# Kernel tuning notes

Measured on AMD Instinct MI355X. Metric: run time of the kernel, lower is better.

The kernel has to match this reference:

```python
import jax, jax.numpy as jnp
import numpy as np

BATCH, SEQ, HIDDEN = 8, 2048, 2048
N_FREQS = SEQ // 2 + 1  # 1025


def setup_inputs() -> dict:
    key = jax.random.key(0)
    k_x, k_w, k_b = jax.random.split(key, 3)
    x = jax.random.normal(k_x, (BATCH, SEQ, HIDDEN), dtype=jnp.float32)
    # Params per __init__: gate init ones/zeros; Linear(hidden, hidden)
    gate_real = jnp.ones((N_FREQS, HIDDEN), dtype=jnp.float32)
    gate_imag = jnp.zeros((N_FREQS, HIDDEN), dtype=jnp.float32)
    bound = 1.0 / np.sqrt(HIDDEN)
    W = jax.random.uniform(k_w, (HIDDEN, HIDDEN), minval=-bound, maxval=bound, dtype=jnp.float32)
    b = jax.random.uniform(k_b, (HIDDEN,), minval=-bound, maxval=bound, dtype=jnp.float32)
    return {"x": x, "gate_real": gate_real, "gate_imag": gate_imag, "W": W, "b": b}


def reference(x, gate_real, gate_imag, W, b):
    # x: (batch, seq, hidden)
    seq_len = x.shape[1]
    x_fft = jnp.fft.rfft(x, axis=1)  # (batch, n_freqs, hidden) complex64
    n_freqs = x_fft.shape[1]
    gate = gate_real[:n_freqs] + 1j * gate_imag[:n_freqs]  # (n_freqs, hidden)
    x_fft = x_fft * gate
    y = jnp.fft.irfft(x_fft, n=seq_len, axis=1)  # (batch, seq, hidden) float32
    # out_proj: y @ W.T + b  (torch Linear convention, W: (out, in))
    out = jnp.einsum('bsh,oh->bso', y, W) + b
    return out
```

## Files before the change

### kernel.cpp

```cpp
#include <hip/hip_runtime.h>
#include <math.h>

typedef __attribute__((ext_vector_type(8))) short bf16x8;
typedef __attribute__((ext_vector_type(4))) float f32x4;

__device__ __forceinline__ unsigned short f2bf(float f) {
  unsigned int u = __float_as_uint(f);
  unsigned int r = (u + 0x7fffu + ((u >> 16) & 1u)) >> 16;
  return (unsigned short)r;
}
__device__ __forceinline__ unsigned int pack2bf(float a, float b) {
  return (unsigned int)f2bf(a) | ((unsigned int)f2bf(b) << 16);
}
__device__ __forceinline__ float bflo(unsigned int g) { return __uint_as_float(g << 16); }
__device__ __forceinline__ float bfhi(unsigned int g) { return __uint_as_float(g & 0xffff0000u); }

__device__ __forceinline__ void glds16(const void* gp, void* lp) {
  __builtin_amdgcn_global_load_lds(
      (const __attribute__((address_space(1))) void*)gp,
      (__attribute__((address_space(3))) void*)lp, 16, 0, 0);
}

__device__ __constant__ float CW16[16] = {
  1.0f, 0.9807852804032304f, 0.9238795325112867f, 0.8314696123025452f,
  0.7071067811865476f, 0.5555702330196022f, 0.3826834323650898f, 0.19509032201612828f,
  0.0f, -0.19509032201612828f, -0.3826834323650898f, -0.5555702330196022f,
  -0.7071067811865476f, -0.8314696123025452f, -0.9238795325112867f, -0.9807852804032304f};
__device__ __constant__ float SW16[16] = {
  0.0f, 0.19509032201612828f, 0.3826834323650898f, 0.5555702330196022f,
  0.7071067811865476f, 0.8314696123025452f, 0.9238795325112867f, 0.9807852804032304f,
  1.0f, 0.9807852804032304f, 0.9238795325112867f, 0.8314696123025452f,
  0.7071067811865476f, 0.5555702330196022f, 0.3826834323650898f, 0.19509032201612828f};
__device__ __constant__ int BR5[32] = {
  0,16,8,24,4,20,12,28,2,18,10,26,6,22,14,30,
  1,17,9,25,5,21,13,29,3,19,11,27,7,23,15,31};

__device__ __forceinline__ int bitrev6(int l) {
  return ((l&1)<<5)|((l&2)<<3)|((l&4)<<1)|((l&8)>>1)|((l&16)>>3)|((l&32)>>5);
}

__device__ __forceinline__ float hsin(float rev) { return __builtin_amdgcn_sinf(rev); }
__device__ __forceinline__ float hcos(float rev) { return __builtin_amdgcn_cosf(rev); }

__device__ __forceinline__ void fwd_core(float (&ur)[32], float (&ui)[32], const int lane) {
  #pragma unroll
  for (int s = 0; s < 6; ++s) {
    const int h = 32 >> s;
    const int j = lane & (h - 1);
    const float rev = (float)j * (0.5f / (float)h);
    const bool hi = (lane & h) != 0;
    const float c  = hi ? hcos(rev) : 1.0f;
    const float sv = hi ? hsin(rev) : 0.0f;
    const float sgn = hi ? -1.0f : 1.0f;
    #pragma unroll
    for (int r = 0; r < 32; ++r) {
      float pr = __shfl_xor(ur[r], h, 64);
      float pi = __shfl_xor(ui[r], h, 64);
      float tr = fmaf(sgn, ur[r], pr);
      float ti = fmaf(sgn, ui[r], pi);
      ur[r] = fmaf(ti, sv, tr * c);
      ui[r] = fmaf(-tr, sv, ti * c);
    }
  }
  const int kap = bitrev6(lane);
  #pragma unroll
  for (int j = 1; j < 32; ++j) {
    const float rev = (float)(j * kap) * (1.0f / 2048.0f);
    const float sn = hsin(rev), cs = hcos(rev);
    float t = ur[j] * cs + ui[j] * sn;
    ui[j] = ui[j] * cs - ur[j] * sn;
    ur[j] = t;
  }
  #pragma unroll
  for (int s = 0; s < 5; ++s) {
    const int h = 16 >> s;
    #pragma unroll
    for (int i = 0; i < 32; ++i) if (!(i & h)) {
      const int tw = (i & (h - 1)) * (16 / h);
      float dr = ur[i] - ur[i + h], di = ui[i] - ui[i + h];
      ur[i] += ur[i + h]; ui[i] += ui[i + h];
      ur[i + h] = dr * CW16[tw] + di * SW16[tw];
      ui[i + h] = di * CW16[tw] - dr * SW16[tw];
    }
  }
}

__device__ __forceinline__ void inv_core(float (&ur)[32], float (&ui)[32], const int lane) {
  const int kap = bitrev6(lane);
  #pragma unroll
  for (int s = 0; s < 5; ++s) {
    const int h = 1 << s;
    #pragma unroll
    for (int i = 0; i < 32; ++i) if (!(i & h)) {
      const int tw = (i & (h - 1)) * (16 / h);
      float tr2 = ur[i + h] * CW16[tw] - ui[i + h] * SW16[tw];
      float ti2 = ui[i + h] * CW16[tw] + ur[i + h] * SW16[tw];
      ur[i + h] = ur[i] - tr2; ui[i + h] = ui[i] - ti2;
      ur[i] += tr2; ui[i] += ti2;
    }
  }
  #pragma unroll
  for (int j = 1; j < 32; ++j) {
    const float rev = (float)(j * kap) * (1.0f / 2048.0f);
    const float sn = hsin(rev), cs = hcos(rev);
    float t = ur[j] * cs - ui[j] * sn;
    ui[j] = ui[j] * cs + ur[j] * sn;
    ur[j] = t;
  }
  #pragma unroll
  for (int s = 0; s < 6; ++s) {
    const int h = 1 << s;
    const int j = lane & (h - 1);
    const float rev = (float)j * (0.5f / (float)h);
    const bool hi = (lane & h) != 0;
    const float c  = hi ? hcos(rev) : 1.0f;
    const float sv = hi ? hsin(rev) : 0.0f;
    const float sgn = hi ? -1.0f : 1.0f;
    #pragma unroll
    for (int r = 0; r < 32; ++r) {
      float vr = fmaf(-ui[r], sv, ur[r] * c);
      float vi = fmaf(ur[r], sv, ui[r] * c);
      float pvr = __shfl_xor(vr, h, 64);
      float pvi = __shfl_xor(vi, h, 64);
      ur[r] = fmaf(sgn, vr, pvr);
      ui[r] = fmaf(sgn, vi, pvi);
    }
  }
}

__global__ __launch_bounds__(256) void gate_pack_k(const float* __restrict__ gr,
                                                   const float* __restrict__ gi,
                                                   unsigned int* __restrict__ gt) {
  __shared__ float tr[32][33];
  __shared__ float ti[32][33];
  const int t = threadIdx.x;
  const int k0 = blockIdx.x * 32, hb = blockIdx.y * 32;
  const int hx = t & 31, fr = t >> 5;
  #pragma unroll
  for (int p = 0; p < 4; ++p) {
    int ff = p * 8 + fr;
    int k = k0 + ff;
    int f = (k <= 1024) ? k : (2048 - k);
    float sg = (k <= 1024) ? 1.f : -1.f;
    tr[ff][hx] = gr[(size_t)f * 2048 + hb + hx] * (1.f / 2048.f);
    ti[ff][hx] = sg * gi[(size_t)f * 2048 + hb + hx] * (1.f / 2048.f);
  }
  __syncthreads();
  const int kk = t & 31, hr = t >> 5;
  #pragma unroll
  for (int p = 0; p < 4; ++p) {
    int hl = p * 8 + hr;
    float re = tr[kk][hl], im = ti[kk][hl];
    gt[(size_t)(hb + hl) * 2048 + k0 + kk] =
        (unsigned int)f2bf(re) | ((unsigned int)f2bf(im) << 16);
  }
}

__global__ __launch_bounds__(256) void gate_ab_k(const float* __restrict__ gr,
                                                 const float* __restrict__ gi,
                                                 uint2* __restrict__ ab) {
  __shared__ unsigned int uA[32][33];
  __shared__ unsigned int uB[32][33];
  const int t = threadIdx.x;
  const int k0 = blockIdx.x * 32, h0 = blockIdx.y * 32;
  const int c = t & 31, r = t >> 5;
  #pragma unroll
  for (int pp = 0; pp < 4; ++pp) {
    const int kk = pp * 8 + r;
    const int k = k0 + kk;
    const int h = h0 + c;
    const float gkr = gr[(size_t)k * 2048 + h];
    const float gki = gi[(size_t)k * 2048 + h];
    const float gcr = gr[(size_t)(1024 - k) * 2048 + h];
    const float gci = gi[(size_t)(1024 - k) * 2048 + h];
    const float inv = 1.0f / 1024.0f;
    float Ar, Ai, Br, Bi;
    if (k == 0) {
      Ar = (gkr + gcr) * 0.5f * inv; Ai = 0.f;
      Br = 0.f; Bi = (gkr - gcr) * 0.5f * inv;
    } else {
      const float rev = (float)k * (1.0f / 2048.0f);
      const float sn = hsin(rev), cs = hcos(rev);
      const float Sr = (gkr + gcr) * 0.5f, Si = (gki - gci) * 0.5f;
      const float Dr = (gkr - gcr) * 0.5f, Di = (gki + gci) * 0.5f;
      Ar = (Sr - sn * Dr) * inv; Ai = (Si - sn * Di) * inv;
      Br = (-cs * Di) * inv;     Bi = (cs * Dr) * inv;
    }
    uA[kk][c] = pack2bf(Ar, Ai);
    uB[kk][c] = pack2bf(Br, Bi);
  }
  __syncthreads();
  #pragma unroll
  for (int pp = 0; pp < 4; ++pp) {
    const int hh = pp * 8 + r;
    ab[(size_t)(h0 + hh) * 1024 + k0 + c] = make_uint2(uA[c][hh], uB[c][hh]);
  }
}

__global__ __launch_bounds__(256) void wconv_k(const float* __restrict__ W,
                                               unsigned short* __restrict__ Wb) {
  int i = blockIdx.x * 256 + threadIdx.x;
  float4 v = ((const float4*)W)[i];
  ushort4 o;
  o.x = f2bf(v.x); o.y = f2bf(v.y); o.z = f2bf(v.z); o.w = f2bf(v.w);
  ((ushort4*)Wb)[i] = o;
}

__global__ __launch_bounds__(256) void xtrans_k(const float* __restrict__ x,
                                                unsigned short* __restrict__ xT) {
  __shared__ float t[64][65];
  const int b = blockIdx.z;
  const int s0 = blockIdx.x * 64, h0 = blockIdx.y * 64;
  const float* xb = x + ((size_t)b * 2048) * 2048;
  unsigned short* xTb = xT + ((size_t)b * 2048) * 2048;
  const int c4 = (threadIdx.x & 15) * 4;
  const int r0 = threadIdx.x >> 4;
  #pragma unroll
  for (int p = 0; p < 4; ++p) {
    const int rr = p * 16 + r0;
    float4 v = *(const float4*)(xb + (size_t)(s0 + rr) * 2048 + h0 + c4);
    t[rr][c4 + 0] = v.x; t[rr][c4 + 1] = v.y;
    t[rr][c4 + 2] = v.z; t[rr][c4 + 3] = v.w;
  }
  __syncthreads();
  const int j = threadIdx.x & 7;
  const int hr0 = threadIdx.x >> 3;
  #pragma unroll
  for (int p = 0; p < 2; ++p) {
    const int hh = p * 32 + hr0;
    uint4 o;
    o.x = pack2bf(t[j * 8 + 0][hh], t[j * 8 + 1][hh]);
    o.y = pack2bf(t[j * 8 + 2][hh], t[j * 8 + 3][hh]);
    o.z = pack2bf(t[j * 8 + 4][hh], t[j * 8 + 5][hh]);
    o.w = pack2bf(t[j * 8 + 6][hh], t[j * 8 + 7][hh]);
    *(uint4*)(xTb + (size_t)(h0 + hh) * 2048 + s0 + j * 8) = o;
  }
}

__global__ __launch_bounds__(256) void ytrans_k(const unsigned short* __restrict__ yT,
                                                unsigned short* __restrict__ y) {
  __shared__ unsigned short t[64][66];
  const int b = blockIdx.z;
  const int h0 = blockIdx.x * 64, s0 = blockIdx.y * 64;
  const unsigned short* src = yT + ((size_t)b * 2048 + h0) * 2048 + s0;
  unsigned short* dst = y + ((size_t)b * 2048 + s0) * 2048 + h0;
  const int c = threadIdx.x & 15, r = threadIdx.x >> 4;
  #pragma unroll
  for (int p = 0; p < 4; ++p) {
    int rr = p * 16 + r;
    ushort4 v = *(const ushort4*)(src + (size_t)rr * 2048 + c * 4);
    *(ushort4*)&t[rr][c * 4] = v;
  }
  __syncthreads();
  #pragma unroll
  for (int p = 0; p < 4; ++p) {
    int rr = p * 16 + r;
    ushort4 o;
    o.x = t[c * 4 + 0][rr]; o.y = t[c * 4 + 1][rr];
    o.z = t[c * 4 + 2][rr]; o.w = t[c * 4 + 3][rr];
    *(ushort4*)(dst + (size_t)rr * 2048 + c * 4) = o;
  }
}

__global__ __attribute__((amdgpu_flat_work_group_size(256, 256)))
__attribute__((amdgpu_waves_per_eu(2, 4)))
void fftr_k(const unsigned short* __restrict__ xT,
            const uint2* __restrict__ ab,
            unsigned short* __restrict__ yT) {
  __shared__ float snap[4][32];
  __shared__ uint2 labs[4][1024];
  const int tid = threadIdx.x;
  const int w = tid >> 6, lane = tid & 63;
  const size_t col = (size_t)blockIdx.x * 4 + w;
  const int h = (int)(col & 2047);
  const int kap = bitrev6(lane);
  constexpr int BR4[16]   = {0,8,4,12,2,10,6,14,1,9,5,13,3,11,7,15};
  constexpr int P0L16[16] = {0,1,3,2,7,6,5,4,15,14,13,12,11,10,9,8};

  {
    const char* gsrc = (const char*)(ab + (size_t)h * 1024);
    char* ldst = (char*)&labs[w][0];
    #pragma unroll
    for (int p8 = 0; p8 < 8; ++p8)
      glds16(gsrc + p8 * 1024 + lane * 16, ldst + p8 * 1024);
  }

  float ur[16], ui[16];
  {
    const unsigned short* xc = xT + col * 2048;
    #pragma unroll
    for (int q = 0; q < 4; ++q) {
      uint4 v = *(const uint4*)(xc + lane * 32 + q * 8);
      ur[4 * q + 0] = bflo(v.x); ui[4 * q + 0] = bfhi(v.x);
      ur[4 * q + 1] = bflo(v.y); ui[4 * q + 1] = bfhi(v.y);
      ur[4 * q + 2] = bflo(v.z); ui[4 * q + 2] = bfhi(v.z);
      ur[4 * q + 3] = bflo(v.w); ui[4 * q + 3] = bfhi(v.w);
    }
  }

  #pragma unroll
  for (int s = 0; s < 6; ++s) {
    const int hh = 32 >> s;
    const int j = lane & (hh - 1);
    const float rev = (float)j * (0.5f / (float)hh);
    const bool hi = (lane & hh) != 0;
    const float c  = hi ? hcos(rev) : 1.0f;
    const float sv = hi ? hsin(rev) : 0.0f;
    const float sgn = hi ? -1.0f : 1.0f;
    #pragma unroll
    for (int r = 0; r < 16; ++r) {
      float pr = __shfl_xor(ur[r], hh, 64);
      float pi = __shfl_xor(ui[r], hh, 64);
      float tr = fmaf(sgn, ur[r], pr);
      float ti = fmaf(sgn, ui[r], pi);
      ur[r] = fmaf(ti, sv, tr * c);
      ui[r] = fmaf(-tr, sv, ti * c);
    }
  }
  #pragma unroll
  for (int j = 1; j < 16; ++j) {
    const float rev = (float)(j * kap) * (1.0f / 1024.0f);
    const float sn = hsin(rev), cs = hcos(rev);
    float t = ur[j] * cs + ui[j] * sn;
    ui[j] = ui[j] * cs - ur[j] * sn;
    ur[j] = t;
  }
  #pragma unroll
  for (int s = 0; s < 4; ++s) {
    const int hh = 8 >> s;
    #pragma unroll
    for (int i = 0; i < 16; ++i) if (!(i & hh)) {
      const int tw = (i & (hh - 1)) * (16 / hh);
      float dr = ur[i] - ur[i + hh], di = ui[i] - ui[i + hh];
      ur[i] += ur[i + hh]; ui[i] += ui[i + hh];
      ur[i + hh] = dr * CW16[tw] + di * SW16[tw];
      ui[i + hh] = di * CW16[tw] - dr * SW16[tw];
    }
  }

  if (lane == 0) {
    #pragma unroll
    for (int p = 0; p < 16; ++p) { snap[w][2 * p] = ur[p]; snap[w][2 * p + 1] = ui[p]; }
  }
  asm volatile("s_waitcnt vmcnt(0)" ::: "memory");
  const int lsrc = bitrev6((64 - kap) & 63);
  const bool l0 = (lane == 0);
  #pragma unroll
  for (int c2 = 0; c2 < 4; ++c2) {
    __builtin_amdgcn_sched_barrier(0);
    #pragma unroll
    for (int pp = 0; pp < 2; ++pp) {
      const int p = c2 * 2 + pp;
      const int pb = 15 - p;
      float arp = __shfl(ur[pb], lsrc), aip = __shfl(ui[pb], lsrc);
      float arq = __shfl(ur[p], lsrc),  aiq = __shfl(ui[p], lsrc);
      float s0r = snap[w][2 * P0L16[p]],  s0i = snap[w][2 * P0L16[p] + 1];
      float s1r = snap[w][2 * P0L16[pb]], s1i = snap[w][2 * P0L16[pb] + 1];
      arp = l0 ? s0r : arp;  aip = l0 ? s0i : aip;
      arq = l0 ? s1r : arq;  aiq = l0 ? s1i : aiq;
      uint2 gp = labs[w][(BR4[p]  << 6) + kap];
      uint2 gq = labs[w][(BR4[pb] << 6) + kap];
      {
        float Ar = bflo(gp.x), Ai = bfhi(gp.x), Br = bflo(gp.y), Bi = bfhi(gp.y);
        float zr = ur[p], zi = ui[p];
        ur[p] = Ar * zr - Ai * zi + Br * arp + Bi * aip;
        ui[p] = Ar * zi + Ai * zr + Bi * arp - Br * aip;
      }
      {
        float Ar = bflo(gq.x), Ai = bfhi(gq.x), Br = bflo(gq.y), Bi = bfhi(gq.y);
        float zr = ur[pb], zi = ui[pb];
        ur[pb] = Ar * zr - Ai * zi + Br * arq + Bi * aiq;
        ui[pb] = Ar * zi + Ai * zr + Bi * arq - Br * aiq;
      }
    }
  }
  __builtin_amdgcn_sched_barrier(0);

  #pragma unroll
  for (int s = 0; s < 4; ++s) {
    const int hh = 1 << s;
    #pragma unroll
    for (int i = 0; i < 16; ++i) if (!(i & hh)) {
      const int tw = (i & (hh - 1)) * (16 / hh);
      float tr2 = ur[i + hh] * CW16[tw] - ui[i + hh] * SW16[tw];
      float ti2 = ui[i + hh] * CW16[tw] + ur[i + hh] * SW16[tw];
      ur[i + hh] = ur[i] - tr2; ui[i + hh] = ui[i] - ti2;
      ur[i] += tr2; ui[i] += ti2;
    }
  }
  #pragma unroll
  for (int j = 1; j < 16; ++j) {
    const float rev = (float)(j * kap) * (1.0f / 1024.0f);
    const float sn = hsin(rev), cs = hcos(rev);
    float t = ur[j] * cs - ui[j] * sn;
    ui[j] = ui[j] * cs + ur[j] * sn;
    ur[j] = t;
  }
  #pragma unroll
  for (int s = 0; s < 6; ++s) {
    const int hh = 1 << s;
    const int j = lane & (hh - 1);
    const float rev = (float)j * (0.5f / (float)hh);
    const bool hi = (lane & hh) != 0;
    const float c  = hi ? hcos(rev) : 1.0f;
    const float sv = hi ? hsin(rev) : 0.0f;
    const float sgn = hi ? -1.0f : 1.0f;
    #pragma unroll
    for (int r = 0; r < 16; ++r) {
      float vr = fmaf(-ui[r], sv, ur[r] * c);
      float vi = fmaf(ur[r], sv, ui[r] * c);
      float pvr = __shfl_xor(vr, hh, 64);
      float pvi = __shfl_xor(vi, hh, 64);
      ur[r] = fmaf(sgn, vr, pvr);
      ui[r] = fmaf(sgn, vi, pvi);
    }
  }

  uint4* dst = (uint4*)(yT + col * 2048) + lane * 4;
  #pragma unroll
  for (int g = 0; g < 4; ++g) {
    uint4 o;
    o.x = pack2bf(ur[4 * g + 0], ui[4 * g + 0]);
    o.y = pack2bf(ur[4 * g + 1], ui[4 * g + 1]);
    o.z = pack2bf(ur[4 * g + 2], ui[4 * g + 2]);
    o.w = pack2bf(ur[4 * g + 3], ui[4 * g + 3]);
    dst[g] = o;
  }
}

__global__ __attribute__((amdgpu_flat_work_group_size(512, 512)))
__attribute__((amdgpu_waves_per_eu(2, 4)))
void fft_gate_k(const float* __restrict__ x,
                const unsigned int* __restrict__ gt,
                unsigned short* __restrict__ y) {
  __shared__ float lds[8 * 516];
  const int tid = threadIdx.x;
  const int w = tid >> 6;
  const int lane = tid & 63;
  const int bid = blockIdx.x;
  const int swz = (bid & 7) * 256 + (bid >> 3);
  const int h0 = (swz & 255) << 3;
  const int b = swz >> 8;
  const int hh = tid & 7, srow = tid >> 3;

  float ur[32], ui[32];
  const size_t xbase = ((size_t)b * 2048) * 2048 + h0;

  for (int c = 0; c < 4; ++c) {
    #pragma unroll
    for (int q = 0; q < 8; ++q) {
      int soff = q * 64 + srow;
      float v = x[xbase + (size_t)(c * 512 + soff) * 2048 + hh];
      lds[hh * 516 + (soff ^ ((soff >> 5) & 15))] = v;
    }
    __syncthreads();
    if ((lane >> 4) == c) {
      const int li = lane & 15;
      #pragma unroll
      for (int j = 0; j < 32; ++j) {
        ur[j] = lds[w * 516 + ((32 * li + j) ^ li)];
        ui[j] = 0.f;
      }
    }
    __syncthreads();
  }

  fwd_core(ur, ui, lane);
  {
    const int kap = bitrev6(lane);
    const unsigned int* grow = gt + (size_t)(h0 + w) * 2048;
    #pragma unroll
    for (int p = 0; p < 32; ++p) {
      unsigned int g = grow[(BR5[p] << 6) + kap];
      float gre = bflo(g), gim = bfhi(g);
      float t = ur[p] * gre - ui[p] * gim;
      ui[p] = ur[p] * gim + ui[p] * gre;
      ur[p] = t;
    }
  }
  inv_core(ur, ui, lane);

  for (int c = 0; c < 4; ++c) {
    if ((lane >> 4) == c) {
      const int li = lane & 15;
      #pragma unroll
      for (int r = 0; r < 32; ++r)
        lds[w * 516 + ((32 * li + r) ^ li)] = ur[r];
    }
    __syncthreads();
    #pragma unroll
    for (int q = 0; q < 8; ++q) {
      int soff = q * 64 + srow;
      float v = lds[hh * 516 + (soff ^ ((soff >> 5) & 15))];
      y[xbase + (size_t)(c * 512 + soff) * 2048 + hh] = f2bf(v);
    }
    __syncthreads();
  }
}

__global__ __launch_bounds__(256) void gemm_k(const unsigned short* __restrict__ A,
                                              const unsigned short* __restrict__ Bw,
                                              const float* __restrict__ bias,
                                              float* __restrict__ C) {
  __shared__ unsigned short sA[128 * 32];
  __shared__ unsigned short sB[128 * 32];
  const int tid = threadIdx.x;
  const int nwg = gridDim.x;
  const int cpx = nwg >> 3;
  const int bid = blockIdx.x;
  const int swz = (bid & 7) * cpx + (bid >> 3);
  const int bm = swz >> 4, bn = swz & 15;
  const int m0 = bm << 7, n0 = bn << 7;
  const int w = tid >> 6, lane = tid & 63;
  const int arow = tid >> 2, koff = (tid & 3) << 3;
  const unsigned short* gA = A + (size_t)(m0 + arow) * 2048 + koff;
  const unsigned short* gB = Bw + (size_t)(n0 + arow) * 2048 + koff;
  char* sAb = (char*)sA + w * 1024;
  char* sBb = (char*)sB + w * 1024;

  f32x4 acc[4][4];
  #pragma unroll
  for (int i = 0; i < 4; ++i)
    #pragma unroll
    for (int j = 0; j < 4; ++j) acc[i][j] = (f32x4){0.f, 0.f, 0.f, 0.f};

  const int wr = w >> 1, wc = w & 1;
  const int row16 = lane & 15, kb = lane >> 4;

  for (int k0 = 0; k0 < 2048; k0 += 32) {
    glds16(gA + k0, sAb);
    glds16(gA + 64 * 2048 + k0, sAb + 4096);
    glds16(gB + k0, sBb);
    glds16(gB + 64 * 2048 + k0, sBb + 4096);
    __syncthreads();
    bf16x8 af[4], bfr[4];
    #pragma unroll
    for (int i = 0; i < 4; ++i) {
      int r = (wr << 6) + (i << 4) + row16;
      af[i] = *(const bf16x8*)(sA + r * 32 + (kb << 3));
    }
    #pragma unroll
    for (int j2 = 0; j2 < 4; ++j2) {
      int r = (wc << 6) + (j2 << 4) + row16;
      bfr[j2] = *(const bf16x8*)(sB + r * 32 + (kb << 3));
    }
    #pragma unroll
    for (int i = 0; i < 4; ++i)
      #pragma unroll
      for (int j2 = 0; j2 < 4; ++j2)
        acc[i][j2] = __builtin_amdgcn_mfma_f32_16x16x32_bf16(af[i], bfr[j2], acc[i][j2], 0, 0, 0);
    __syncthreads();
  }

  const int rq = lane >> 4;
  #pragma unroll
  for (int j2 = 0; j2 < 4; ++j2) {
    int oc = n0 + (wc << 6) + (j2 << 4) + row16;
    float bj = bias[oc];
    #pragma unroll
    for (int i = 0; i < 4; ++i) {
      int mr = m0 + (wr << 6) + (i << 4) + (rq << 2);
      #pragma unroll
      for (int q = 0; q < 4; ++q)
        C[(size_t)(mr + q) * 2048 + oc] = acc[i][j2][q] + bj;
    }
  }
}

__global__ __launch_bounds__(512) void gemm8_k(const unsigned short* __restrict__ A,
                                               const unsigned short* __restrict__ Bw,
                                               const float* __restrict__ bias,
                                               float* __restrict__ C) {
  extern __shared__ char lds[];
  const int tid = threadIdx.x;
  const int w = tid >> 6, lane = tid & 63;
  const int bid = blockIdx.x;
  const int swz = (bid & 7) * 64 + (bid >> 3);
  const int m0 = (swz >> 3) << 8;
  const int n0 = (swz & 7) << 8;
  const int wr = w >> 2, wc = w & 3;
  const int row16 = lane & 15, kb = lane >> 4;

  const int lr = lane >> 2, ls = lane & 3;
  const int r0 = (w << 5) + lr, r1 = r0 + 16;
  const unsigned short* pA0 = A  + (size_t)(m0 + r0) * 2048 + ((ls ^ ((r0 >> 1) & 3)) << 3);
  const unsigned short* pA1 = A  + (size_t)(m0 + r1) * 2048 + ((ls ^ ((r1 >> 1) & 3)) << 3);
  const unsigned short* pB0 = Bw + (size_t)(n0 + r0) * 2048 + ((ls ^ ((r0 >> 1) & 3)) << 3);
  const unsigned short* pB1 = Bw + (size_t)(n0 + r1) * 2048 + ((ls ^ ((r1 >> 1) & 3)) << 3);
  const int dW = w << 11;

  f32x4 acc[8][4];
  #pragma unroll
  for (int i = 0; i < 8; ++i)
    #pragma unroll
    for (int j = 0; j < 4; ++j) acc[i][j] = (f32x4){0.f, 0.f, 0.f, 0.f};

  auto STAGE_A = [&](int t) {
    char* base = lds + ((t & 3) << 15);
    const int k0 = t << 5;
    glds16(pA0 + k0, base + dW);
    glds16(pA1 + k0, base + dW + 1024);
  };
  auto STAGE_B = [&](int t) {
    char* base = lds + ((t & 3) << 15);
    const int k0 = t << 5;
    glds16(pB0 + k0, base + 16384 + dW);
    glds16(pB1 + k0, base + 16384 + dW + 1024);
  };
  auto LDA4 = [&](const char* base, int i0, bf16x8 (&af)[4]) {
    #pragma unroll
    for (int i = 0; i < 4; ++i) {
      const int r = (wr << 7) + ((i0 + i) << 4) + row16;
      af[i] = *(const bf16x8*)(base + (r << 6) + ((kb ^ ((r >> 1) & 3)) << 4));
    }
  };
  auto LDB4 = [&](const char* base, bf16x8 (&bfr)[4]) {
    #pragma unroll
    for (int j = 0; j < 4; ++j) {
      const int r = (wc << 6) + (j << 4) + row16;
      bfr[j] = *(const bf16x8*)(base + 16384 + (r << 6) + ((kb ^ ((r >> 1) & 3)) << 4));
    }
  };
  auto MM16 = [&](const bf16x8 (&af)[4], const bf16x8 (&bfr)[4], int i0) {
    #pragma unroll
    for (int i = 0; i < 4; ++i)
      #pragma unroll
      for (int j = 0; j < 4; ++j)
        acc[i0 + i][j] = __builtin_amdgcn_mfma_f32_16x16x32_bf16(af[i], bfr[j], acc[i0 + i][j], 0, 0, 0);
  };
  auto COMPUTE = [&](int t) {
    const char* base = lds + ((t & 3) << 15);
    bf16x8 af[4], af2[4], bfr[4];
    LDA4(base, 0, af); LDA4(base, 4, af2); LDB4(base, bfr);
    MM16(af, bfr, 0); MM16(af2, bfr, 4);
  };

  STAGE_A(0); STAGE_B(0); STAGE_A(1); STAGE_B(1); STAGE_A(2); STAGE_B(2);
  asm volatile("s_waitcnt vmcnt(8)" ::: "memory");
  __builtin_amdgcn_s_barrier();
  __builtin_amdgcn_sched_barrier(0);

  for (int t = 0; t < 61; ++t) {
    const char* base = lds + ((t & 3) << 15);
    bf16x8 af[4], bfr[4];
    LDA4(base, 0, af);
    LDB4(base, bfr);
    STAGE_A(t + 3);
    asm volatile("s_waitcnt lgkmcnt(0)" ::: "memory");
    __builtin_amdgcn_sched_barrier(0);
    __builtin_amdgcn_s_setprio(1);
    MM16(af, bfr, 0);
    __builtin_amdgcn_s_setprio(0);
    __builtin_amdgcn_s_barrier();
    bf16x8 af2[4];
    LDA4(base, 4, af2);
    STAGE_B(t + 3);
    asm volatile("s_waitcnt lgkmcnt(0)" ::: "memory");
    __builtin_amdgcn_sched_barrier(0);
    __builtin_amdgcn_s_setprio(1);
    MM16(af2, bfr, 4);
    __builtin_amdgcn_s_setprio(0);
    asm volatile("s_waitcnt vmcnt(8)" ::: "memory");
    __builtin_amdgcn_s_barrier();
    __builtin_amdgcn_sched_barrier(0);
  }
  COMPUTE(61);
  asm volatile("s_waitcnt vmcnt(4)" ::: "memory");
  __builtin_amdgcn_s_barrier();
  __builtin_amdgcn_sched_barrier(0);
  COMPUTE(62);
  asm volatile("s_waitcnt vmcnt(0)" ::: "memory");
  __builtin_amdgcn_s_barrier();
  __builtin_amdgcn_sched_barrier(0);
  COMPUTE(63);

  const int rq = lane >> 4;
  #pragma unroll
  for (int j = 0; j < 4; ++j) {
    const int oc = n0 + (wc << 6) + (j << 4) + row16;
    const float bj = bias[oc];
    #pragma unroll
    for (int i = 0; i < 8; ++i) {
      const int mr = m0 + (wr << 7) + (i << 4) + (rq << 2);
      #pragma unroll
      for (int q = 0; q < 4; ++q)
        C[(size_t)(mr + q) * 2048 + oc] = acc[i][j][q] + bj;
    }
  }
}

extern "C" void kernel_launch(void* const* d_in, const int* in_sizes, int n_in,
                              void* d_out, int out_size, void* d_ws, size_t ws_size,
                              hipStream_t stream) {
  const float* x  = (const float*)d_in[0];
  const float* gr = (const float*)d_in[1];
  const float* gi = (const float*)d_in[2];
  const float* W  = (const float*)d_in[3];
  const float* bs = (const float*)d_in[4];
  float* out = (float*)d_out;

  char* ws = (char*)d_ws;
  unsigned short* yb = (unsigned short*)ws;
  unsigned short* Wb = (unsigned short*)(ws + (64ull << 20));
  unsigned int*   gt = (unsigned int*)(ws + (72ull << 20));
  uint2*          ab = (uint2*)(ws + (72ull << 20));
  unsigned short* xT = (unsigned short*)(ws + (88ull << 20));
  unsigned short* yT = (unsigned short*)(ws + (216ull << 20));
  const bool fast = ws_size >= (280ull << 20);

  hipLaunchKernelGGL(wconv_k, dim3(4096), dim3(256), 0, stream, W, Wb);
  if (fast) {
    hipLaunchKernelGGL(gate_ab_k, dim3(32, 64), dim3(256), 0, stream, gr, gi, ab);
    hipLaunchKernelGGL(xtrans_k, dim3(32, 32, 8), dim3(256), 0, stream, x, xT);
    hipLaunchKernelGGL(fftr_k, dim3(4096), dim3(256), 0, stream, xT, ab, yT);
    hipLaunchKernelGGL(ytrans_k, dim3(32, 32, 8), dim3(256), 0, stream, yT, yb);
  } else {
    hipLaunchKernelGGL(gate_pack_k, dim3(64, 64), dim3(256), 0, stream, gr, gi, gt);
    hipLaunchKernelGGL(fft_gate_k, dim3(2048), dim3(512), 0, stream, x, gt, yb);
  }

  const bool big = hipFuncSetAttribute((const void*)gemm8_k,
                                       hipFuncAttributeMaxDynamicSharedMemorySize,
                                       131072) == hipSuccess;
  if (big) {
    hipLaunchKernelGGL(gemm8_k, dim3(512), dim3(512), 131072, stream, yb, Wb, bs, out);
  } else {
    hipLaunchKernelGGL(gemm_k, dim3(2048), dim3(256), 0, stream, yb, Wb, bs, out);
  }
}
```

Baseline: 337.2 us.

## Replace 256x256 8-wave GEMM with 128x256 4-wave tile and 3-stage pipeline

Switches the output-projection GEMM from 512-thread blocks on 256x256 tiles with a 4-deep LDS ring (128 KB) to 256-thread blocks on 128x256 tiles with a 3-stage ring (72 KB), launching 1024 blocks instead of 512. Each wave now computes a 128x64 sub-tile and stages all A and B data for one k-step in a single call. The aim is better CU occupancy and load balance with smaller LDS use, but each tile reuses its operands less, so more global traffic is needed per FLOP, and the prefetch is one stage shallower.

```diff
diff --git a/kernel.cpp b/kernel.cpp
--- a/kernel.cpp
+++ b/kernel.cpp
@@ -567,7 +567,7 @@
   }
 }
 
-__global__ __launch_bounds__(512) void gemm8_k(const unsigned short* __restrict__ A,
+__global__ __launch_bounds__(256) void gemm4_k(const unsigned short* __restrict__ A,
                                                const unsigned short* __restrict__ Bw,
                                                const float* __restrict__ bias,
                                                float* __restrict__ C) {
@@ -575,19 +575,17 @@
   const int tid = threadIdx.x;
   const int w = tid >> 6, lane = tid & 63;
   const int bid = blockIdx.x;
-  const int swz = (bid & 7) * 64 + (bid >> 3);
-  const int m0 = (swz >> 3) << 8;
+  const int swz = (bid & 7) * 128 + (bid >> 3);
+  const int m0 = (swz >> 3) << 7;
   const int n0 = (swz & 7) << 8;
-  const int wr = w >> 2, wc = w & 3;
+  const int wc = w;
   const int row16 = lane & 15, kb = lane >> 4;
 
-  const int lr = lane >> 2, ls = lane & 3;
-  const int r0 = (w << 5) + lr, r1 = r0 + 16;
-  const unsigned short* pA0 = A  + (size_t)(m0 + r0) * 2048 + ((ls ^ ((r0 >> 1) & 3)) << 3);
-  const unsigned short* pA1 = A  + (size_t)(m0 + r1) * 2048 + ((ls ^ ((r1 >> 1) & 3)) << 3);
-  const unsigned short* pB0 = Bw + (size_t)(n0 + r0) * 2048 + ((ls ^ ((r0 >> 1) & 3)) << 3);
-  const unsigned short* pB1 = Bw + (size_t)(n0 + r1) * 2048 + ((ls ^ ((r1 >> 1) & 3)) << 3);
-  const int dW = w << 11;
+  const int rs = (w << 4) + (lane >> 2);
+  const int sseg = (lane & 3) ^ ((rs >> 1) & 3);
+  const unsigned short* pA = A  + (size_t)(m0 + rs) * 2048 + (sseg << 3);
+  const unsigned short* pB = Bw + (size_t)(n0 + rs) * 2048 + (sseg << 3);
+  const int dW = w << 10;
 
   f32x4 acc[8][4];
   #pragma unroll
@@ -595,22 +593,20 @@
     #pragma unroll
     for (int j = 0; j < 4; ++j) acc[i][j] = (f32x4){0.f, 0.f, 0.f, 0.f};
 
-  auto STAGE_A = [&](int t) {
-    char* base = lds + ((t & 3) << 15);
+  auto STAGE = [&](int t) {
+    char* base = lds + (t % 3) * 24576;
     const int k0 = t << 5;
-    glds16(pA0 + k0, base + dW);
-    glds16(pA1 + k0, base + dW + 1024);
-  };
-  auto STAGE_B = [&](int t) {
-    char* base = lds + ((t & 3) << 15);
-    const int k0 = t << 5;
-    glds16(pB0 + k0, base + 16384 + dW);
-    glds16(pB1 + k0, base + 16384 + dW + 1024);
+    glds16(pA + k0, base + dW);
+    glds16(pA + 64 * 2048 + k0, base + 4096 + dW);
+    glds16(pB + k0, base + 8192 + dW);
+    glds16(pB + 64 * 2048 + k0, base + 12288 + dW);
+    glds16(pB + 128 * 2048 + k0, base + 16384 + dW);
+    glds16(pB + 192 * 2048 + k0, base + 20480 + dW);
   };
   auto LDA4 = [&](const char* base, int i0, bf16x8 (&af)[4]) {
     #pragma unroll
     for (int i = 0; i < 4; ++i) {
-      const int r = (wr << 7) + ((i0 + i) << 4) + row16;
+      const int r = ((i0 + i) << 4) + row16;
       af[i] = *(const bf16x8*)(base + (r << 6) + ((kb ^ ((r >> 1) & 3)) << 4));
     }
   };
@@ -618,7 +614,7 @@
     #pragma unroll
     for (int j = 0; j < 4; ++j) {
       const int r = (wc << 6) + (j << 4) + row16;
-      bfr[j] = *(const bf16x8*)(base + 16384 + (r << 6) + ((kb ^ ((r >> 1) & 3)) << 4));
+      bfr[j] = *(const bf16x8*)(base + 8192 + (r << 6) + ((kb ^ ((r >> 1) & 3)) << 4));
     }
   };
   auto MM16 = [&](const bf16x8 (&af)[4], const bf16x8 (&bfr)[4], int i0) {
@@ -628,24 +624,18 @@
       for (int j = 0; j < 4; ++j)
         acc[i0 + i][j] = __builtin_amdgcn_mfma_f32_16x16x32_bf16(af[i], bfr[j], acc[i0 + i][j], 0, 0, 0);
   };
-  auto COMPUTE = [&](int t) {
-    const char* base = lds + ((t & 3) << 15);
-    bf16x8 af[4], af2[4], bfr[4];
-    LDA4(base, 0, af); LDA4(base, 4, af2); LDB4(base, bfr);
-    MM16(af, bfr, 0); MM16(af2, bfr, 4);
-  };
-
-  STAGE_A(0); STAGE_B(0); STAGE_A(1); STAGE_B(1); STAGE_A(2); STAGE_B(2);
-  asm volatile("s_waitcnt vmcnt(8)" ::: "memory");
+
+  STAGE(0); STAGE(1);
+  asm volatile("s_waitcnt vmcnt(6)" ::: "memory");
   __builtin_amdgcn_s_barrier();
   __builtin_amdgcn_sched_barrier(0);
 
-  for (int t = 0; t < 61; ++t) {
-    const char* base = lds + ((t & 3) << 15);
+  for (int t = 0; t < 62; ++t) {
+    const char* base = lds + (t % 3) * 24576;
     bf16x8 af[4], bfr[4];
     LDA4(base, 0, af);
     LDB4(base, bfr);
-    STAGE_A(t + 3);
+    STAGE(t + 2);
     asm volatile("s_waitcnt lgkmcnt(0)" ::: "memory");
     __builtin_amdgcn_sched_barrier(0);
     __builtin_amdgcn_s_setprio(1);
@@ -654,25 +644,30 @@
     __builtin_amdgcn_s_barrier();
     bf16x8 af2[4];
     LDA4(base, 4, af2);
-    STAGE_B(t + 3);
     asm volatile("s_waitcnt lgkmcnt(0)" ::: "memory");
     __builtin_amdgcn_sched_barrier(0);
     __builtin_amdgcn_s_setprio(1);
     MM16(af2, bfr, 4);
     __builtin_amdgcn_s_setprio(0);
-    asm volatile("s_waitcnt vmcnt(8)" ::: "memory");
+    asm volatile("s_waitcnt vmcnt(6)" ::: "memory");
     __builtin_amdgcn_s_barrier();
     __builtin_amdgcn_sched_barrier(0);
   }
-  COMPUTE(61);
-  asm volatile("s_waitcnt vmcnt(4)" ::: "memory");
-  __builtin_amdgcn_s_barrier();
-  __builtin_amdgcn_sched_barrier(0);
-  COMPUTE(62);
-  asm volatile("s_waitcnt vmcnt(0)" ::: "memory");
-  __builtin_amdgcn_s_barrier();
-  __builtin_amdgcn_sched_barrier(0);
-  COMPUTE(63);
+  {
+    const char* base = lds + (62 % 3) * 24576;
+    bf16x8 af[4], af2[4], bfr[4];
+    LDA4(base, 0, af); LDA4(base, 4, af2); LDB4(base, bfr);
+    MM16(af, bfr, 0); MM16(af2, bfr, 4);
+    asm volatile("s_waitcnt vmcnt(0)" ::: "memory");
+    __builtin_amdgcn_s_barrier();
+    __builtin_amdgcn_sched_barrier(0);
+  }
+  {
+    const char* base = lds + (63 % 3) * 24576;
+    bf16x8 af[4], af2[4], bfr[4];
+    LDA4(base, 0, af); LDA4(base, 4, af2); LDB4(base, bfr);
+    MM16(af, bfr, 0); MM16(af2, bfr, 4);
+  }
 
   const int rq = lane >> 4;
   #pragma unroll
@@ -681,7 +676,7 @@
     const float bj = bias[oc];
     #pragma unroll
     for (int i = 0; i < 8; ++i) {
-      const int mr = m0 + (wr << 7) + (i << 4) + (rq << 2);
+      const int mr = m0 + (i << 4) + (rq << 2);
       #pragma unroll
       for (int q = 0; q < 4; ++q)
         C[(size_t)(mr + q) * 2048 + oc] = acc[i][j][q] + bj;
@@ -719,11 +714,11 @@
     hipLaunchKernelGGL(fft_gate_k, dim3(2048), dim3(512), 0, stream, x, gt, yb);
   }
 
-  const bool big = hipFuncSetAttribute((const void*)gemm8_k,
+  const bool big = hipFuncSetAttribute((const void*)gemm4_k,
                                        hipFuncAttributeMaxDynamicSharedMemorySize,
-                                       131072) == hipSuccess;
+                                       73728) == hipSuccess;
   if (big) {
-    hipLaunchKernelGGL(gemm8_k, dim3(512), dim3(512), 131072, stream, yb, Wb, bs, out);
+    hipLaunchKernelGGL(gemm4_k, dim3(1024), dim3(256), 73728, stream, yb, Wb, bs, out);
   } else {
     hipLaunchKernelGGL(gemm_k, dim3(2048), dim3(256), 0, stream, yb, Wb, bs, out);
   }
```

New measurement: 404.7 us. +20.0%, slower.
